# Kernel tuning notes

Hardware: AMD Instinct MI355X
Metric: run time of the kernel (lower is better)

Reference implementation:

```python
import jax, jax.numpy as jnp
import numpy as np

INPUT_SIZE = 40960
HIDDEN = 256
BATCH = 32768
ACTIVE = 32  # active features per position (~one per piece)


def setup_inputs() -> dict:
    key = jax.random.key(0)
    ks = jax.random.split(key, 11)
    return {
        "white_idx": jax.random.randint(ks[0], (BATCH, ACTIVE), 0, INPUT_SIZE, dtype=jnp.int32),
        "black_idx": jax.random.randint(ks[1], (BATCH, ACTIVE), 0, INPUT_SIZE, dtype=jnp.int32),
        "stm": jax.random.randint(ks[2], (BATCH, 1), 0, 2).astype(jnp.float32),
        "ft_w": jax.random.normal(ks[3], (INPUT_SIZE, HIDDEN), dtype=jnp.float32) * 0.02,
        "ft_b": jax.random.normal(ks[4], (HIDDEN,), dtype=jnp.float32) * 0.02,
        "l1_w": jax.random.normal(ks[5], (32, 2 * HIDDEN), dtype=jnp.float32) * 0.05,
        "l1_b": jax.random.normal(ks[6], (32,), dtype=jnp.float32) * 0.05,
        "l2_w": jax.random.normal(ks[7], (32, 32), dtype=jnp.float32) * 0.05,
        "l2_b": jax.random.normal(ks[8], (32,), dtype=jnp.float32) * 0.05,
        "l3_w": jax.random.normal(ks[9], (1, 32), dtype=jnp.float32) * 0.05,
        "l3_b": jax.random.normal(ks[10], (1,), dtype=jnp.float32) * 0.05,
    }


def _ft(idx, ft_w, ft_b):
    # sparse-COO (unit values) @ ft.weight^T + bias == gather rows of the
    # [input_size, hidden] table and sum over active features.
    return ft_w[idx].sum(axis=1) + ft_b  # [B, H]


def reference(white_idx, black_idx, stm, ft_w, ft_b, l1_w, l1_b, l2_w, l2_b, l3_w, l3_b):
    w = jnp.clip(_ft(white_idx, ft_w, ft_b), 0.0, 1.0)
    b = jnp.clip(_ft(black_idx, ft_w, ft_b), 0.0, 1.0)
    acc = stm * jnp.concatenate([w, b], axis=1) + (1.0 - stm) * jnp.concatenate([b, w], axis=1)
    x = jnp.clip(acc @ l1_w.T + l1_b, 0.0, 1.0)
    x = jnp.clip(x @ l2_w.T + l2_b, 0.0, 1.0)
    return x @ l3_w.T + l3_b  # [B, 1]
```

## Files before the change

kernel.cpp:

```cpp
#include <hip/hip_runtime.h>

#define BATCH 32768
#define HID 256
#define ACT 32
#define NROWS 40960

#define TBL_BYTES ((size_t)NROWS * HID * 2)
#define ACT_BYTES ((size_t)BATCH * 512 * 4)

__global__ __launch_bounds__(256) void nnue_cvt_kernel(
    const float* __restrict__ ft_w, unsigned short* __restrict__ tbl)
{
    const int g  = blockIdx.y;
    const int tx = blockIdx.x * 256 + threadIdx.x;
    const int row = tx >> 2;
    const int c8  = tx & 3;
    const float* __restrict__ src = ft_w + (size_t)row * HID + g * 32 + c8 * 8;
    unsigned int o[8];
    #pragma unroll
    for (int j = 0; j < 8; ++j) {
        unsigned int u = __float_as_uint(src[j]);
        u = u + 0x7FFFu + ((u >> 16) & 1u);
        o[j] = u >> 16;
    }
    uint4 pack;
    pack.x = o[0] | (o[1] << 16);
    pack.y = o[2] | (o[3] << 16);
    pack.z = o[4] | (o[5] << 16);
    pack.w = o[6] | (o[7] << 16);
    *(uint4*)(tbl + ((size_t)g * NROWS + row) * 32 + c8 * 8) = pack;
}

#define LDU2(o) (*(const uint2*)(tg + (unsigned int)(o) + cb))

__global__ __launch_bounds__(256, 8) void nnue_ft_kernel(
    const int* __restrict__ widx, const int* __restrict__ bidx,
    const float* __restrict__ stm,
    const unsigned short* __restrict__ tbl, const float* __restrict__ ft_b,
    float* __restrict__ act)
{
    const int bid = blockIdx.x;
    const int g   = bid & 7;
    const int pt  = bid >> 3;
    const int t   = threadIdx.x;
    const int q   = t & 63;
    const int p   = (t >> 6) * 8 + (q >> 3);
    const int c   = q & 7;

    __shared__ int   soff[32][68];
    __shared__ float sstm[32];

    #pragma unroll
    for (int k = 0; k < 4; ++k) {
        const int u  = t + k * 256;
        const int pp = u >> 5, rr = u & 31;
        soff[pp][rr]      = widx[(size_t)(pt * 32 + pp) * ACT + rr] << 6;
        soff[pp][32 + rr] = bidx[(size_t)(pt * 32 + pp) * ACT + rr] << 6;
    }
    if (t < 32) sstm[t] = stm[pt * 32 + t];
    __syncthreads();

    const char* __restrict__ tg = (const char*)(tbl + (size_t)g * NROWS * 32);
    const unsigned int cb = (unsigned int)(c << 3);
    const int4* __restrict__ sview = (const int4*)(&soff[p][0]);

    float a0=0.f,a1=0.f,a2=0.f,a3=0.f;
    float b0=0.f,b1=0.f,b2=0.f,b3=0.f;

    #pragma unroll
    for (int blk = 0; blk < 4; ++blk) {
        const int4 oA = sview[blk * 2];
        const int4 oB = sview[blk * 2 + 1];
        uint2 v[8];
        v[0] = LDU2(oA.x); v[1] = LDU2(oA.y); v[2] = LDU2(oA.z); v[3] = LDU2(oA.w);
        v[4] = LDU2(oB.x); v[5] = LDU2(oB.y); v[6] = LDU2(oB.z); v[7] = LDU2(oB.w);
        #pragma unroll
        for (int i = 0; i < 8; ++i) {
            a0 += __uint_as_float(v[i].x << 16);
            a1 += __uint_as_float(v[i].x & 0xFFFF0000u);
            a2 += __uint_as_float(v[i].y << 16);
            a3 += __uint_as_float(v[i].y & 0xFFFF0000u);
        }
    }
    #pragma unroll
    for (int blk = 4; blk < 8; ++blk) {
        const int4 oA = sview[blk * 2];
        const int4 oB = sview[blk * 2 + 1];
        uint2 v[8];
        v[0] = LDU2(oA.x); v[1] = LDU2(oA.y); v[2] = LDU2(oA.z); v[3] = LDU2(oA.w);
        v[4] = LDU2(oB.x); v[5] = LDU2(oB.y); v[6] = LDU2(oB.z); v[7] = LDU2(oB.w);
        #pragma unroll
        for (int i = 0; i < 8; ++i) {
            b0 += __uint_as_float(v[i].x << 16);
            b1 += __uint_as_float(v[i].x & 0xFFFF0000u);
            b2 += __uint_as_float(v[i].y << 16);
            b3 += __uint_as_float(v[i].y & 0xFFFF0000u);
        }
    }

    const float4 bv = ((const float4*)ft_b)[g * 8 + c];
    float4 wa, za;
    wa.x = fminf(fmaxf(a0 + bv.x, 0.f), 1.f);
    wa.y = fminf(fmaxf(a1 + bv.y, 0.f), 1.f);
    wa.z = fminf(fmaxf(a2 + bv.z, 0.f), 1.f);
    wa.w = fminf(fmaxf(a3 + bv.w, 0.f), 1.f);
    za.x = fminf(fmaxf(b0 + bv.x, 0.f), 1.f);
    za.y = fminf(fmaxf(b1 + bv.y, 0.f), 1.f);
    za.z = fminf(fmaxf(b2 + bv.z, 0.f), 1.f);
    za.w = fminf(fmaxf(b3 + bv.w, 0.f), 1.f);

    const int  pos = pt * 32 + p;
    const bool s   = (sstm[p] != 0.0f);
    float* dst = act + (size_t)pos * 512 + g * 32 + (c << 2);
    *(float4*)(dst + (s ? 0 : 256)) = wa;
    *(float4*)(dst + (s ? 256 : 0)) = za;
}

__global__ __launch_bounds__(256, 4) void nnue_mlp_kernel(
    const float* __restrict__ act,
    const float* __restrict__ l1_w, const float* __restrict__ l1_b,
    const float* __restrict__ l2_w, const float* __restrict__ l2_b,
    const float* __restrict__ l3_w, const float* __restrict__ l3_b,
    float* __restrict__ out)
{
    const int bb = blockIdx.x;
    const int t  = threadIdx.x;

    __shared__ float4 sact[16 * 128];
    __shared__ float  x1s[16][33];
    __shared__ float  x2s[16][33];

    const float4* __restrict__ ga = (const float4*)(act + (size_t)bb * 16 * 512);
    #pragma unroll
    for (int k = 0; k < 8; ++k) sact[t + k * 256] = ga[t + k * 256];
    __syncthreads();

    {
        const int o  = t >> 3;
        const int l8 = t & 7;
        const float4* __restrict__ wrow = (const float4*)(l1_w + o * 512);
        float pacc[16];
        #pragma unroll
        for (int p = 0; p < 16; ++p) pacc[p] = 0.f;
        #pragma unroll
        for (int j = 0; j < 16; ++j) {
            const int i4 = l8 + j * 8;
            const float4 wv = wrow[i4];
            #pragma unroll
            for (int p = 0; p < 16; ++p) {
                const float4 a = sact[p * 128 + i4];
                pacc[p] += wv.x*a.x + wv.y*a.y + wv.z*a.z + wv.w*a.w;
            }
        }
        #pragma unroll
        for (int p = 0; p < 16; ++p) {
            pacc[p] += __shfl_down(pacc[p], 4, 8);
            pacc[p] += __shfl_down(pacc[p], 2, 8);
            pacc[p] += __shfl_down(pacc[p], 1, 8);
        }
        if (l8 == 0) {
            const float bo = l1_b[o];
            #pragma unroll
            for (int p = 0; p < 16; ++p)
                x1s[p][o] = fminf(fmaxf(pacc[p] + bo, 0.f), 1.f);
        }
    }
    __syncthreads();

    #pragma unroll
    for (int h = 0; h < 2; ++h) {
        const int p  = h * 8 + (t >> 5);
        const int oo = t & 31;
        const float* __restrict__ wr = l2_w + oo * 32;
        float s2 = l2_b[oo];
        #pragma unroll
        for (int j = 0; j < 32; ++j) s2 += x1s[p][j] * wr[j];
        x2s[p][oo] = fminf(fmaxf(s2, 0.f), 1.f);
    }
    __syncthreads();

    if (t < 16) {
        float s3 = l3_b[0];
        #pragma unroll
        for (int j = 0; j < 32; ++j) s3 += x2s[t][j] * l3_w[j];
        out[bb * 16 + t] = s3;
    }
}

__device__ __forceinline__ float4 clip4(float4 v) {
    v.x = fminf(fmaxf(v.x, 0.0f), 1.0f);
    v.y = fminf(fmaxf(v.y, 0.0f), 1.0f);
    v.z = fminf(fmaxf(v.z, 0.0f), 1.0f);
    v.w = fminf(fmaxf(v.w, 0.0f), 1.0f);
    return v;
}
__device__ __forceinline__ void acc4(float4& a, const float4 v) {
    a.x += v.x; a.y += v.y; a.z += v.z; a.w += v.w;
}

__global__ __launch_bounds__(256, 4) void nnue_fwd_fallback(
    const int* __restrict__ widx, const int* __restrict__ bidx,
    const float* __restrict__ stm,
    const float* __restrict__ ft_w, const float* __restrict__ ft_b,
    const float* __restrict__ l1_w, const float* __restrict__ l1_b,
    const float* __restrict__ l2_w, const float* __restrict__ l2_b,
    const float* __restrict__ l3_w, const float* __restrict__ l3_b,
    float* __restrict__ out)
{
    const int bb = blockIdx.x;
    const int t  = threadIdx.x;
    const int w  = t >> 6;
    const int q  = t & 63;

    __shared__ float4 accbuf[4][128];
    __shared__ float  x1s[4][32];
    __shared__ float  x2s[4][32];

    const int pos = bb * 4 + w;
    int myidx;
    if (q < 32) myidx = widx[pos * ACT + q];
    else        myidx = bidx[pos * ACT + (q - 32)];

    const float4* __restrict__ ftw4 = (const float4*)ft_w;
    const float4  bias = ((const float4*)ft_b)[q];
    float4 accW = bias, accB = bias;

    #pragma unroll
    for (int r0 = 0; r0 < 32; r0 += 8) {
        float4 vw[8], vb[8];
        #pragma unroll
        for (int i = 0; i < 8; ++i) {
            const int rw = __builtin_amdgcn_readlane(myidx, r0 + i);
            vw[i] = ftw4[(size_t)rw * 64 + q];
        }
        #pragma unroll
        for (int i = 0; i < 8; ++i) {
            const int rb = __builtin_amdgcn_readlane(myidx, 32 + r0 + i);
            vb[i] = ftw4[(size_t)rb * 64 + q];
        }
        #pragma unroll
        for (int i = 0; i < 8; ++i) { acc4(accW, vw[i]); acc4(accB, vb[i]); }
    }

    const bool s = (stm[pos] != 0.0f);
    accbuf[w][(s ? 0 : 64) + q] = clip4(accW);
    accbuf[w][(s ? 64 : 0) + q] = clip4(accB);
    __syncthreads();

    {
        const int o  = t >> 3;
        const int l8 = t & 7;
        const float4* __restrict__ wrow = (const float4*)(l1_w + o * 512);
        float p0 = 0.f, p1 = 0.f, p2 = 0.f, p3 = 0.f;
        #pragma unroll
        for (int j = 0; j < 16; ++j) {
            const int i4 = l8 + j * 8;
            const float4 wv = wrow[i4];
            const float4 a0 = accbuf[0][i4];
            const float4 a1 = accbuf[1][i4];
            const float4 a2 = accbuf[2][i4];
            const float4 a3 = accbuf[3][i4];
            p0 += wv.x*a0.x + wv.y*a0.y + wv.z*a0.z + wv.w*a0.w;
            p1 += wv.x*a1.x + wv.y*a1.y + wv.z*a1.z + wv.w*a1.w;
            p2 += wv.x*a2.x + wv.y*a2.y + wv.z*a2.z + wv.w*a2.w;
            p3 += wv.x*a3.x + wv.y*a3.y + wv.z*a3.z + wv.w*a3.w;
        }
        p0 += __shfl_down(p0, 4, 8); p0 += __shfl_down(p0, 2, 8); p0 += __shfl_down(p0, 1, 8);
        p1 += __shfl_down(p1, 4, 8); p1 += __shfl_down(p1, 2, 8); p1 += __shfl_down(p1, 1, 8);
        p2 += __shfl_down(p2, 4, 8); p2 += __shfl_down(p2, 2, 8); p2 += __shfl_down(p2, 1, 8);
        p3 += __shfl_down(p3, 4, 8); p3 += __shfl_down(p3, 2, 8); p3 += __shfl_down(p3, 1, 8);
        if (l8 == 0) {
            const float bo = l1_b[o];
            x1s[0][o] = fminf(fmaxf(p0 + bo, 0.0f), 1.0f);
            x1s[1][o] = fminf(fmaxf(p1 + bo, 0.0f), 1.0f);
            x1s[2][o] = fminf(fmaxf(p2 + bo, 0.0f), 1.0f);
            x1s[3][o] = fminf(fmaxf(p3 + bo, 0.0f), 1.0f);
        }
    }
    __syncthreads();

    if (t < 128) {
        const int g  = t >> 5;
        const int oo = t & 31;
        const float* __restrict__ wr = l2_w + oo * 32;
        float p = l2_b[oo];
        #pragma unroll
        for (int j = 0; j < 32; ++j) p += x1s[g][j] * wr[j];
        x2s[g][oo] = fminf(fmaxf(p, 0.0f), 1.0f);
    }
    __syncthreads();

    if (t < 4) {
        float p = l3_b[0];
        #pragma unroll
        for (int j = 0; j < 32; ++j) p += x2s[t][j] * l3_w[j];
        out[bb * 4 + t] = p;
    }
}

extern "C" void kernel_launch(void* const* d_in, const int* in_sizes, int n_in,
                              void* d_out, int out_size, void* d_ws, size_t ws_size,
                              hipStream_t stream) {
    const int*   widx = (const int*)d_in[0];
    const int*   bidx = (const int*)d_in[1];
    const float* stm  = (const float*)d_in[2];
    const float* ft_w = (const float*)d_in[3];
    const float* ft_b = (const float*)d_in[4];
    const float* l1_w = (const float*)d_in[5];
    const float* l1_b = (const float*)d_in[6];
    const float* l2_w = (const float*)d_in[7];
    const float* l2_b = (const float*)d_in[8];
    const float* l3_w = (const float*)d_in[9];
    const float* l3_b = (const float*)d_in[10];
    float* out = (float*)d_out;

    if (ws_size >= TBL_BYTES + ACT_BYTES) {
        unsigned short* tbl = (unsigned short*)d_ws;
        float* act = (float*)((char*)d_ws + TBL_BYTES);
        nnue_cvt_kernel<<<dim3(640, 8), 256, 0, stream>>>(ft_w, tbl);
        nnue_ft_kernel<<<(BATCH / 32) * 8, 256, 0, stream>>>(widx, bidx, stm, tbl, ft_b, act);
        nnue_mlp_kernel<<<BATCH / 16, 256, 0, stream>>>(act, l1_w, l1_b, l2_w, l2_b, l3_w, l3_b, out);
    } else {
        nnue_fwd_fallback<<<BATCH / 4, 256, 0, stream>>>(
            widx, bidx, stm, ft_w, ft_b, l1_w, l1_b, l2_w, l2_b, l3_w, l3_b, out);
    }
}
```

Measured before the change: 151.4 us.

## Widen bf16 table slabs to 64 columns with 16-byte gathers; halve MLP tile

The bf16 feature table is re-laid out into 4 column slabs of 64 instead of 8 slabs of 32. Each feature-transformer thread now gathers 16 bytes per row and accumulates 8 columns, which halves the number of blocks and the redundant index loading. Occupancy hints drop from 8 to 6 to leave room for the extra registers. The MLP kernel now handles 8 positions per block instead of 16, doubling the grid and cutting registers and shared memory per block, at the cost of more l1_w reloads.

```diff
diff --git a/kernel.cpp b/kernel.cpp
--- a/kernel.cpp
+++ b/kernel.cpp
@@ -13,9 +13,9 @@
 {
     const int g  = blockIdx.y;
     const int tx = blockIdx.x * 256 + threadIdx.x;
-    const int row = tx >> 2;
-    const int c8  = tx & 3;
-    const float* __restrict__ src = ft_w + (size_t)row * HID + g * 32 + c8 * 8;
+    const int row = tx >> 3;
+    const int c8  = tx & 7;
+    const float* __restrict__ src = ft_w + (size_t)row * HID + g * 64 + c8 * 8;
     unsigned int o[8];
     #pragma unroll
     for (int j = 0; j < 8; ++j) {
@@ -28,24 +28,34 @@
     pack.y = o[2] | (o[3] << 16);
     pack.z = o[4] | (o[5] << 16);
     pack.w = o[6] | (o[7] << 16);
-    *(uint4*)(tbl + ((size_t)g * NROWS + row) * 32 + c8 * 8) = pack;
-}
-
-#define LDU2(o) (*(const uint2*)(tg + (unsigned int)(o) + cb))
-
-__global__ __launch_bounds__(256, 8) void nnue_ft_kernel(
+    *(uint4*)(tbl + ((size_t)g * NROWS + row) * 64 + c8 * 8) = pack;
+}
+
+#define LDU4(o) (*(const uint4*)(tg + (unsigned int)(o) + cb))
+
+__device__ __forceinline__ void acc8(float* a, const uint4 v) {
+    a[0] += __uint_as_float(v.x << 16);
+    a[1] += __uint_as_float(v.x & 0xFFFF0000u);
+    a[2] += __uint_as_float(v.y << 16);
+    a[3] += __uint_as_float(v.y & 0xFFFF0000u);
+    a[4] += __uint_as_float(v.z << 16);
+    a[5] += __uint_as_float(v.z & 0xFFFF0000u);
+    a[6] += __uint_as_float(v.w << 16);
+    a[7] += __uint_as_float(v.w & 0xFFFF0000u);
+}
+
+__global__ __launch_bounds__(256, 6) void nnue_ft_kernel(
     const int* __restrict__ widx, const int* __restrict__ bidx,
     const float* __restrict__ stm,
     const unsigned short* __restrict__ tbl, const float* __restrict__ ft_b,
     float* __restrict__ act)
 {
     const int bid = blockIdx.x;
-    const int g   = bid & 7;
-    const int pt  = bid >> 3;
+    const int g   = bid & 3;
+    const int pt  = bid >> 2;
     const int t   = threadIdx.x;
-    const int q   = t & 63;
-    const int p   = (t >> 6) * 8 + (q >> 3);
-    const int c   = q & 7;
+    const int p   = t >> 3;
+    const int c   = t & 7;
 
     __shared__ int   soff[32][68];
     __shared__ float sstm[32];
@@ -54,66 +64,68 @@
     for (int k = 0; k < 4; ++k) {
         const int u  = t + k * 256;
         const int pp = u >> 5, rr = u & 31;
-        soff[pp][rr]      = widx[(size_t)(pt * 32 + pp) * ACT + rr] << 6;
-        soff[pp][32 + rr] = bidx[(size_t)(pt * 32 + pp) * ACT + rr] << 6;
+        soff[pp][rr]      = widx[(size_t)(pt * 32 + pp) * ACT + rr] << 7;
+        soff[pp][32 + rr] = bidx[(size_t)(pt * 32 + pp) * ACT + rr] << 7;
     }
     if (t < 32) sstm[t] = stm[pt * 32 + t];
     __syncthreads();
 
-    const char* __restrict__ tg = (const char*)(tbl + (size_t)g * NROWS * 32);
-    const unsigned int cb = (unsigned int)(c << 3);
+    const char* __restrict__ tg = (const char*)tbl + (size_t)g * NROWS * 128;
+    const unsigned int cb = (unsigned int)(c << 4);
     const int4* __restrict__ sview = (const int4*)(&soff[p][0]);
 
-    float a0=0.f,a1=0.f,a2=0.f,a3=0.f;
-    float b0=0.f,b1=0.f,b2=0.f,b3=0.f;
+    float wa[8] = {0.f,0.f,0.f,0.f,0.f,0.f,0.f,0.f};
+    float ba[8] = {0.f,0.f,0.f,0.f,0.f,0.f,0.f,0.f};
 
     #pragma unroll
     for (int blk = 0; blk < 4; ++blk) {
         const int4 oA = sview[blk * 2];
         const int4 oB = sview[blk * 2 + 1];
-        uint2 v[8];
-        v[0] = LDU2(oA.x); v[1] = LDU2(oA.y); v[2] = LDU2(oA.z); v[3] = LDU2(oA.w);
-        v[4] = LDU2(oB.x); v[5] = LDU2(oB.y); v[6] = LDU2(oB.z); v[7] = LDU2(oB.w);
-        #pragma unroll
-        for (int i = 0; i < 8; ++i) {
-            a0 += __uint_as_float(v[i].x << 16);
-            a1 += __uint_as_float(v[i].x & 0xFFFF0000u);
-            a2 += __uint_as_float(v[i].y << 16);
-            a3 += __uint_as_float(v[i].y & 0xFFFF0000u);
-        }
+        uint4 v[8];
+        v[0] = LDU4(oA.x); v[1] = LDU4(oA.y); v[2] = LDU4(oA.z); v[3] = LDU4(oA.w);
+        v[4] = LDU4(oB.x); v[5] = LDU4(oB.y); v[6] = LDU4(oB.z); v[7] = LDU4(oB.w);
+        #pragma unroll
+        for (int i = 0; i < 8; ++i) acc8(wa, v[i]);
     }
     #pragma unroll
     for (int blk = 4; blk < 8; ++blk) {
         const int4 oA = sview[blk * 2];
         const int4 oB = sview[blk * 2 + 1];
-        uint2 v[8];
-        v[0] = LDU2(oA.x); v[1] = LDU2(oA.y); v[2] = LDU2(oA.z); v[3] = LDU2(oA.w);
-        v[4] = LDU2(oB.x); v[5] = LDU2(oB.y); v[6] = LDU2(oB.z); v[7] = LDU2(oB.w);
-        #pragma unroll
-        for (int i = 0; i < 8; ++i) {
-            b0 += __uint_as_float(v[i].x << 16);
-            b1 += __uint_as_float(v[i].x & 0xFFFF0000u);
-            b2 += __uint_as_float(v[i].y << 16);
-            b3 += __uint_as_float(v[i].y & 0xFFFF0000u);
-        }
-    }
-
-    const float4 bv = ((const float4*)ft_b)[g * 8 + c];
-    float4 wa, za;
-    wa.x = fminf(fmaxf(a0 + bv.x, 0.f), 1.f);
-    wa.y = fminf(fmaxf(a1 + bv.y, 0.f), 1.f);
-    wa.z = fminf(fmaxf(a2 + bv.z, 0.f), 1.f);
-    wa.w = fminf(fmaxf(a3 + bv.w, 0.f), 1.f);
-    za.x = fminf(fmaxf(b0 + bv.x, 0.f), 1.f);
-    za.y = fminf(fmaxf(b1 + bv.y, 0.f), 1.f);
-    za.z = fminf(fmaxf(b2 + bv.z, 0.f), 1.f);
-    za.w = fminf(fmaxf(b3 + bv.w, 0.f), 1.f);
+        uint4 v[8];
+        v[0] = LDU4(oA.x); v[1] = LDU4(oA.y); v[2] = LDU4(oA.z); v[3] = LDU4(oA.w);
+        v[4] = LDU4(oB.x); v[5] = LDU4(oB.y); v[6] = LDU4(oB.z); v[7] = LDU4(oB.w);
+        #pragma unroll
+        for (int i = 0; i < 8; ++i) acc8(ba, v[i]);
+    }
+
+    const float4 bv0 = ((const float4*)ft_b)[g * 16 + c * 2];
+    const float4 bv1 = ((const float4*)ft_b)[g * 16 + c * 2 + 1];
+
+    float4 w0, w1, z0, z1;
+    w0.x = fminf(fmaxf(wa[0] + bv0.x, 0.f), 1.f);
+    w0.y = fminf(fmaxf(wa[1] + bv0.y, 0.f), 1.f);
+    w0.z = fminf(fmaxf(wa[2] + bv0.z, 0.f), 1.f);
+    w0.w = fminf(fmaxf(wa[3] + bv0.w, 0.f), 1.f);
+    w1.x = fminf(fmaxf(wa[4] + bv1.x, 0.f), 1.f);
+    w1.y = fminf(fmaxf(wa[5] + bv1.y, 0.f), 1.f);
+    w1.z = fminf(fmaxf(wa[6] + bv1.z, 0.f), 1.f);
+    w1.w = fminf(fmaxf(wa[7] + bv1.w, 0.f), 1.f);
+    z0.x = fminf(fmaxf(ba[0] + bv0.x, 0.f), 1.f);
+    z0.y = fminf(fmaxf(ba[1] + bv0.y, 0.f), 1.f);
+    z0.z = fminf(fmaxf(ba[2] + bv0.z, 0.f), 1.f);
+    z0.w = fminf(fmaxf(ba[3] + bv0.w, 0.f), 1.f);
+    z1.x = fminf(fmaxf(ba[4] + bv1.x, 0.f), 1.f);
+    z1.y = fminf(fmaxf(ba[5] + bv1.y, 0.f), 1.f);
+    z1.z = fminf(fmaxf(ba[6] + bv1.z, 0.f), 1.f);
+    z1.w = fminf(fmaxf(ba[7] + bv1.w, 0.f), 1.f);
 
     const int  pos = pt * 32 + p;
     const bool s   = (sstm[p] != 0.0f);
-    float* dst = act + (size_t)pos * 512 + g * 32 + (c << 2);
-    *(float4*)(dst + (s ? 0 : 256)) = wa;
-    *(float4*)(dst + (s ? 256 : 0)) = za;
+    float* dst = act + (size_t)pos * 512 + g * 64 + c * 8;
+    *(float4*)(dst     + (s ? 0 : 256)) = w0;
+    *(float4*)(dst + 4 + (s ? 0 : 256)) = w1;
+    *(float4*)(dst     + (s ? 256 : 0)) = z0;
+    *(float4*)(dst + 4 + (s ? 256 : 0)) = z1;
 }
 
 __global__ __launch_bounds__(256, 4) void nnue_mlp_kernel(
@@ -126,34 +138,32 @@
     const int bb = blockIdx.x;
     const int t  = threadIdx.x;
 
-    __shared__ float4 sact[16 * 128];
-    __shared__ float  x1s[16][33];
-    __shared__ float  x2s[16][33];
-
-    const float4* __restrict__ ga = (const float4*)(act + (size_t)bb * 16 * 512);
-    #pragma unroll
-    for (int k = 0; k < 8; ++k) sact[t + k * 256] = ga[t + k * 256];
+    __shared__ float4 sact[8 * 128];
+    __shared__ float  x1s[8][33];
+    __shared__ float  x2s[8][33];
+
+    const float4* __restrict__ ga = (const float4*)(act + (size_t)bb * 8 * 512);
+    #pragma unroll
+    for (int k = 0; k < 4; ++k) sact[t + k * 256] = ga[t + k * 256];
     __syncthreads();
 
     {
         const int o  = t >> 3;
         const int l8 = t & 7;
         const float4* __restrict__ wrow = (const float4*)(l1_w + o * 512);
-        float pacc[16];
-        #pragma unroll
-        for (int p = 0; p < 16; ++p) pacc[p] = 0.f;
+        float pacc[8] = {0.f,0.f,0.f,0.f,0.f,0.f,0.f,0.f};
         #pragma unroll
         for (int j = 0; j < 16; ++j) {
             const int i4 = l8 + j * 8;
             const float4 wv = wrow[i4];
             #pragma unroll
-            for (int p = 0; p < 16; ++p) {
+            for (int p = 0; p < 8; ++p) {
                 const float4 a = sact[p * 128 + i4];
                 pacc[p] += wv.x*a.x + wv.y*a.y + wv.z*a.z + wv.w*a.w;
             }
         }
         #pragma unroll
-        for (int p = 0; p < 16; ++p) {
+        for (int p = 0; p < 8; ++p) {
             pacc[p] += __shfl_down(pacc[p], 4, 8);
             pacc[p] += __shfl_down(pacc[p], 2, 8);
             pacc[p] += __shfl_down(pacc[p], 1, 8);
@@ -161,15 +171,14 @@
         if (l8 == 0) {
             const float bo = l1_b[o];
             #pragma unroll
-            for (int p = 0; p < 16; ++p)
+            for (int p = 0; p < 8; ++p)
                 x1s[p][o] = fminf(fmaxf(pacc[p] + bo, 0.f), 1.f);
         }
     }
     __syncthreads();
 
-    #pragma unroll
-    for (int h = 0; h < 2; ++h) {
-        const int p  = h * 8 + (t >> 5);
+    {
+        const int p  = t >> 5;
         const int oo = t & 31;
         const float* __restrict__ wr = l2_w + oo * 32;
         float s2 = l2_b[oo];
@@ -179,11 +188,11 @@
     }
     __syncthreads();
 
-    if (t < 16) {
+    if (t < 8) {
         float s3 = l3_b[0];
         #pragma unroll
         for (int j = 0; j < 32; ++j) s3 += x2s[t][j] * l3_w[j];
-        out[bb * 16 + t] = s3;
+        out[bb * 8 + t] = s3;
     }
 }
 
@@ -317,9 +326,9 @@
     if (ws_size >= TBL_BYTES + ACT_BYTES) {
         unsigned short* tbl = (unsigned short*)d_ws;
         float* act = (float*)((char*)d_ws + TBL_BYTES);
-        nnue_cvt_kernel<<<dim3(640, 8), 256, 0, stream>>>(ft_w, tbl);
-        nnue_ft_kernel<<<(BATCH / 32) * 8, 256, 0, stream>>>(widx, bidx, stm, tbl, ft_b, act);
-        nnue_mlp_kernel<<<BATCH / 16, 256, 0, stream>>>(act, l1_w, l1_b, l2_w, l2_b, l3_w, l3_b, out);
+        nnue_cvt_kernel<<<dim3(1280, 4), 256, 0, stream>>>(ft_w, tbl);
+        nnue_ft_kernel<<<(BATCH / 32) * 4, 256, 0, stream>>>(widx, bidx, stm, tbl, ft_b, act);
+        nnue_mlp_kernel<<<BATCH / 8, 256, 0, stream>>>(act, l1_w, l1_b, l2_w, l2_b, l3_w, l3_b, out);
     } else {
         nnue_fwd_fallback<<<BATCH / 4, 256, 0, stream>>>(
             widx, bidx, stm, ft_w, ft_b, l1_w, l1_b, l2_w, l2_b, l3_w, l3_b, out);
```

Result: slower. 181.7 us (+20.0%).
